# Kernel optimization log

Hardware: AMD Instinct MI355X
Metric: run time of the kernel (lower is better)

## Reference

```python
import jax, jax.numpy as jnp
import numpy as np

B, T, E, H = 2, 1024, 1024, 16
HD = E // H
TEMP = 0.5


def setup_inputs() -> dict:
    key = jax.random.key(0)
    ks = jax.random.split(key, 20)
    d = {
        "query1": jax.random.normal(ks[0], (B, T, E), jnp.float32),
        "query2": jax.random.normal(ks[1], (B, T, E), jnp.float32),
        "key": jax.random.normal(ks[2], (B, T, E), jnp.float32),
        "value": jax.random.normal(ks[3], (B, T, E), jnp.float32),
    }
    s = 1.0 / np.sqrt(E)
    names = ["Wq", "Wq2", "Wq3", "Wk", "Wv", "Wo"]
    for i, n in enumerate(names):
        d[n] = jax.random.normal(ks[4 + i], (E, E), jnp.float32) * s
        d["b" + n[1:]] = jax.random.normal(ks[10 + i], (E,), jnp.float32) * 0.01
    return d


def _heads(x):
    # [B,T,E] -> [B,H,T,HD]
    b, t, _ = x.shape
    return x.reshape(b, t, H, HD).transpose(0, 2, 1, 3)


def reference(query1, query2, key, value,
              Wq, bq, Wq2, bq2, Wq3, bq3, Wk, bk, Wv, bv, Wo, bo):
    q = _heads(query1 @ Wq.T + bq)
    q2 = _heads(query2 @ Wq2.T + bq2)
    q3 = _heads(key @ Wq3.T + bq3)
    k = _heads(key @ Wk.T + bk)
    v = _heads(value @ Wv.T + bv)
    b, _, t, _ = q.shape
    scale = 1.0 / np.sqrt(HD)

    def global_attn(qx):
        s = jnp.einsum('bhtd,bhsd->bhts', qx, k) * scale  # [B,H,T,T]
        # global softmax over flattened T*T, temperature-scaled, times T
        a = jax.nn.softmax((s / TEMP).reshape(b, H, t * t), axis=-1)
        return a.reshape(b, H, t, t) * t

    a1 = global_attn(q)
    a2 = global_attn(q2)
    a3 = global_attn(q3)
    attn_out = jnp.einsum('bhts,bhsd->bthd', (a1 + a2 + a3) / 3.0, v)
    attn_out = attn_out.reshape(b, t, E)
    output = attn_out @ Wo.T + bo
    return output, a1
```

## Files before the change

kernel.cpp:

```cpp
#include <hip/hip_runtime.h>
#include <hip/hip_bf16.h>


#define B_ 2
#define T_ 1024
#define E_ 1024
#define H_ 16
#define HD_ 64
#define BH_ 32

typedef float f32x4 __attribute__((ext_vector_type(4)));
typedef short bfrag __attribute__((ext_vector_type(8)));

__device__ __forceinline__ unsigned short f2b(float f) {
  unsigned int u = __float_as_uint(f);
  u += 0x7fffu + ((u >> 16) & 1u);
  return (unsigned short)(u >> 16);
}

struct CvtArgs { const float* src[10]; unsigned short* dst[10]; int n[10]; };

__global__ __launch_bounds__(256) void cvt_kernel(CvtArgs a) {
  const int z = blockIdx.y;
  const float* __restrict__ s = a.src[z];
  unsigned short* __restrict__ d = a.dst[z];
  const int n = a.n[z];
  const int stride = gridDim.x * 256 * 4;
  for (int i = (blockIdx.x * 256 + threadIdx.x) * 4; i < n; i += stride) {
    float4 v = *(const float4*)(s + i);
    ushort4 o;
    o.x = f2b(v.x); o.y = f2b(v.y); o.z = f2b(v.z); o.w = f2b(v.w);
    *(ushort4*)(d + i) = o;
  }
}

__device__ __forceinline__ void mm128_core(const unsigned short* __restrict__ A,
                                           const unsigned short* __restrict__ W,
                                           int m0, int n0,
                                           unsigned short* As, unsigned short* Bs,
                                           f32x4 acc[4][4]) {
  const int tid  = threadIdx.x;
  const int lane = tid & 63, w = tid >> 6;
  const int lrow = lane & 15, quad = lane >> 4;
  const int wm = (w >> 1) * 64, wn = (w & 1) * 64;
  const int srow = tid >> 2, soff = (tid & 3) * 8;

  const unsigned short* Ar0 = A + (size_t)(m0 + srow) * E_ + soff;
  const unsigned short* Ar1 = Ar0 + (size_t)64 * E_;
  const unsigned short* Br0 = W + (size_t)(n0 + srow) * E_ + soff;
  const unsigned short* Br1 = Br0 + (size_t)64 * E_;

  for (int k0 = 0; k0 < E_; k0 += 32) {
    int4 a0 = *(const int4*)(Ar0 + k0);
    int4 a1 = *(const int4*)(Ar1 + k0);
    int4 b0 = *(const int4*)(Br0 + k0);
    int4 b1 = *(const int4*)(Br1 + k0);
    __syncthreads();
    *(int4*)(As + srow * 32 + soff)        = a0;
    *(int4*)(As + (srow + 64) * 32 + soff) = a1;
    *(int4*)(Bs + srow * 32 + soff)        = b0;
    *(int4*)(Bs + (srow + 64) * 32 + soff) = b1;
    __syncthreads();
    bfrag af[4], bf_[4];
#pragma unroll
    for (int mt = 0; mt < 4; mt++)
      af[mt] = *(const bfrag*)(As + (wm + mt * 16 + lrow) * 32 + quad * 8);
#pragma unroll
    for (int nt = 0; nt < 4; nt++)
      bf_[nt] = *(const bfrag*)(Bs + (wn + nt * 16 + lrow) * 32 + quad * 8);
#pragma unroll
    for (int mt = 0; mt < 4; mt++)
#pragma unroll
      for (int nt = 0; nt < 4; nt++)
        acc[mt][nt] = __builtin_amdgcn_mfma_f32_16x16x32_bf16(af[mt], bf_[nt], acc[mt][nt], 0, 0, 0);
  }
}

struct ProjArgs {
  const unsigned short* X[5];
  const unsigned short* W[5];
  const float* bias[5];
  unsigned short* dst[5];
};

__global__ __launch_bounds__(256) void proj_kernel(ProjArgs pa) {
  __shared__ unsigned short As[128 * 32];
  __shared__ unsigned short Bs[128 * 32];
  const int z = blockIdx.z;
  const int m0 = blockIdx.y * 128, n0 = blockIdx.x * 128;
  f32x4 acc[4][4];
#pragma unroll
  for (int mt = 0; mt < 4; mt++)
#pragma unroll
    for (int nt = 0; nt < 4; nt++) acc[mt][nt] = (f32x4)0.f;

  mm128_core(pa.X[z], pa.W[z], m0, n0, As, Bs, acc);

  const int tid = threadIdx.x, lane = tid & 63, w = tid >> 6;
  const int lrow = lane & 15, quad = lane >> 4;
  const int wm = (w >> 1) * 64, wn = (w & 1) * 64;
  const float* __restrict__ bias = pa.bias[z];
  unsigned short* __restrict__ dst = pa.dst[z];
  float bv[4];
#pragma unroll
  for (int nt = 0; nt < 4; nt++) bv[nt] = bias[n0 + wn + nt * 16 + lrow];
#pragma unroll
  for (int mt = 0; mt < 4; mt++)
#pragma unroll
    for (int nt = 0; nt < 4; nt++)
#pragma unroll
      for (int ii = 0; ii < 4; ii++) {
        const int m = m0 + wm + mt * 16 + quad * 4 + ii;
        const int n = n0 + wn + nt * 16 + lrow;
        const float v = acc[mt][nt][ii] + bv[nt];
        const int b = m >> 10, t = m & 1023, h = n >> 6, dd = n & 63;
        size_t idx;
        if (z == 4)
          idx = ((size_t)((b * H_ + h) * HD_ + dd)) * T_ + t;
        else
          idx = ((size_t)((b * H_ + h) * T_ + t)) * HD_ + dd;
        dst[idx] = f2b(v);
      }
}

__global__ __launch_bounds__(256) void attn_sums_kernel(
    const unsigned short* __restrict__ Q1, const unsigned short* __restrict__ Q2,
    const unsigned short* __restrict__ Q3, const unsigned short* __restrict__ Kh,
    float* __restrict__ sums) {
  const int tid = threadIdx.x, lane = tid & 63, w = tid >> 6;
  const int lrow = lane & 15, quad = lane >> 4;
  const int tw = w >> 1, sw = w & 1;
  const int bh = blockIdx.y;
  const int tb = blockIdx.x * 128 + tw * 64;
  const size_t base = (size_t)bh * T_ * HD_;
  const unsigned short* Qs[3] = {Q1 + base, Q2 + base, Q3 + base};
  const unsigned short* Kb = Kh + base;

  float lsum[3] = {0.f, 0.f, 0.f};
  for (int s0 = 0; s0 < T_; s0 += 128) {
    const int sb = s0 + sw * 64;
#pragma unroll
    for (int i = 0; i < 3; i++) {
      f32x4 acc[4][4];
#pragma unroll
      for (int mt = 0; mt < 4; mt++)
#pragma unroll
        for (int nt = 0; nt < 4; nt++) acc[mt][nt] = (f32x4)0.f;
#pragma unroll
      for (int kk = 0; kk < 2; kk++) {
        bfrag af[4], bf_[4];
#pragma unroll
        for (int mt = 0; mt < 4; mt++)
          af[mt] = *(const bfrag*)(Qs[i] + (size_t)(tb + mt * 16 + lrow) * HD_ + kk * 32 + quad * 8);
#pragma unroll
        for (int nt = 0; nt < 4; nt++)
          bf_[nt] = *(const bfrag*)(Kb + (size_t)(sb + nt * 16 + lrow) * HD_ + kk * 32 + quad * 8);
#pragma unroll
        for (int mt = 0; mt < 4; mt++)
#pragma unroll
          for (int nt = 0; nt < 4; nt++)
            acc[mt][nt] = __builtin_amdgcn_mfma_f32_16x16x32_bf16(af[mt], bf_[nt], acc[mt][nt], 0, 0, 0);
      }
      float s = 0.f;
#pragma unroll
      for (int mt = 0; mt < 4; mt++)
#pragma unroll
        for (int nt = 0; nt < 4; nt++)
#pragma unroll
          for (int ii = 0; ii < 4; ii++)
            s += __expf(acc[mt][nt][ii] * 0.25f);
      lsum[i] += s;
    }
  }
#pragma unroll
  for (int i = 0; i < 3; i++) {
    float v = lsum[i];
    for (int off = 32; off > 0; off >>= 1) v += __shfl_down(v, off, 64);
    if (lane == 0) atomicAdd(&sums[i * BH_ + bh], v);
  }
}

__global__ __launch_bounds__(256) void attn_main_kernel(
    const unsigned short* __restrict__ Q1, const unsigned short* __restrict__ Q2,
    const unsigned short* __restrict__ Q3, const unsigned short* __restrict__ Kh,
    const unsigned short* __restrict__ Vt, const float* __restrict__ sums,
    float* __restrict__ a1out, unsigned short* __restrict__ attn_out) {
  __shared__ unsigned short P[128 * 136];
  const int tid = threadIdx.x, lane = tid & 63, w = tid >> 6;
  const int lrow = lane & 15, quad = lane >> 4;
  const int tw = w >> 1, sw = w & 1, dw = sw;
  const int bh = blockIdx.y;
  const int b = bh >> 4, h = bh & 15;
  const int tb = blockIdx.x * 128 + tw * 64;
  const size_t base = (size_t)bh * T_ * HD_;
  const unsigned short* Qs[3] = {Q1 + base, Q2 + base, Q3 + base};
  const unsigned short* Kb = Kh + base;
  const unsigned short* Vb = Vt + (size_t)bh * HD_ * T_;

  float r[3];
#pragma unroll
  for (int i = 0; i < 3; i++) r[i] = (float)T_ / (3.f * sums[i * BH_ + bh]);
  const float a1s = 3.f * r[0];

  f32x4 oacc[4][2];
#pragma unroll
  for (int mt = 0; mt < 4; mt++) { oacc[mt][0] = (f32x4)0.f; oacc[mt][1] = (f32x4)0.f; }

  for (int s0 = 0; s0 < T_; s0 += 128) {
    const int sb = s0 + sw * 64;
    f32x4 pc[4][4];
#pragma unroll
    for (int mt = 0; mt < 4; mt++)
#pragma unroll
      for (int nt = 0; nt < 4; nt++) pc[mt][nt] = (f32x4)0.f;

#pragma unroll
    for (int i = 0; i < 3; i++) {
      f32x4 acc[4][4];
#pragma unroll
      for (int mt = 0; mt < 4; mt++)
#pragma unroll
        for (int nt = 0; nt < 4; nt++) acc[mt][nt] = (f32x4)0.f;
#pragma unroll
      for (int kk = 0; kk < 2; kk++) {
        bfrag af[4], bf_[4];
#pragma unroll
        for (int mt = 0; mt < 4; mt++)
          af[mt] = *(const bfrag*)(Qs[i] + (size_t)(tb + mt * 16 + lrow) * HD_ + kk * 32 + quad * 8);
#pragma unroll
        for (int nt = 0; nt < 4; nt++)
          bf_[nt] = *(const bfrag*)(Kb + (size_t)(sb + nt * 16 + lrow) * HD_ + kk * 32 + quad * 8);
#pragma unroll
        for (int mt = 0; mt < 4; mt++)
#pragma unroll
          for (int nt = 0; nt < 4; nt++)
            acc[mt][nt] = __builtin_amdgcn_mfma_f32_16x16x32_bf16(af[mt], bf_[nt], acc[mt][nt], 0, 0, 0);
      }
      const float ri = r[i];
#pragma unroll
      for (int mt = 0; mt < 4; mt++)
#pragma unroll
        for (int nt = 0; nt < 4; nt++)
#pragma unroll
          for (int ii = 0; ii < 4; ii++) {
            const float e = __expf(acc[mt][nt][ii] * 0.25f);
            pc[mt][nt][ii] += ri * e;
            if (i == 0) {
              const int t = tb + mt * 16 + quad * 4 + ii;
              const int s = sb + nt * 16 + lrow;
              a1out[((size_t)bh * T_ + t) * T_ + s] = e * a1s;
            }
          }
    }
    __syncthreads();
#pragma unroll
    for (int mt = 0; mt < 4; mt++)
#pragma unroll
      for (int nt = 0; nt < 4; nt++)
#pragma unroll
        for (int ii = 0; ii < 4; ii++) {
          const int tl = tw * 64 + mt * 16 + quad * 4 + ii;
          const int sl = sw * 64 + nt * 16 + lrow;
          P[tl * 136 + sl] = f2b(pc[mt][nt][ii]);
        }
    __syncthreads();
#pragma unroll
    for (int kk = 0; kk < 4; kk++) {
      bfrag pf[4], vf[2];
#pragma unroll
      for (int mt = 0; mt < 4; mt++)
        pf[mt] = *(const bfrag*)(P + (tw * 64 + mt * 16 + lrow) * 136 + kk * 32 + quad * 8);
#pragma unroll
      for (int nt = 0; nt < 2; nt++)
        vf[nt] = *(const bfrag*)(Vb + (size_t)(dw * 32 + nt * 16 + lrow) * T_ + s0 + kk * 32 + quad * 8);
#pragma unroll
      for (int mt = 0; mt < 4; mt++)
#pragma unroll
        for (int nt = 0; nt < 2; nt++)
          oacc[mt][nt] = __builtin_amdgcn_mfma_f32_16x16x32_bf16(pf[mt], vf[nt], oacc[mt][nt], 0, 0, 0);
    }
  }
#pragma unroll
  for (int mt = 0; mt < 4; mt++)
#pragma unroll
    for (int nt = 0; nt < 2; nt++)
#pragma unroll
      for (int ii = 0; ii < 4; ii++) {
        const int t = tb + mt * 16 + quad * 4 + ii;
        const int dd = dw * 32 + nt * 16 + lrow;
        attn_out[((size_t)(b * T_ + t)) * E_ + h * HD_ + dd] = f2b(oacc[mt][nt][ii]);
      }
}

__global__ __launch_bounds__(256) void outproj_kernel(
    const unsigned short* __restrict__ Ab, const unsigned short* __restrict__ Wb,
    const float* __restrict__ bias, float* __restrict__ out) {
  __shared__ unsigned short As[128 * 32];
  __shared__ unsigned short Bs[128 * 32];
  const int m0 = blockIdx.y * 128, n0 = blockIdx.x * 128;
  f32x4 acc[4][4];
#pragma unroll
  for (int mt = 0; mt < 4; mt++)
#pragma unroll
    for (int nt = 0; nt < 4; nt++) acc[mt][nt] = (f32x4)0.f;

  mm128_core(Ab, Wb, m0, n0, As, Bs, acc);

  const int tid = threadIdx.x, lane = tid & 63, w = tid >> 6;
  const int lrow = lane & 15, quad = lane >> 4;
  const int wm = (w >> 1) * 64, wn = (w & 1) * 64;
  float bv[4];
#pragma unroll
  for (int nt = 0; nt < 4; nt++) bv[nt] = bias[n0 + wn + nt * 16 + lrow];
#pragma unroll
  for (int mt = 0; mt < 4; mt++)
#pragma unroll
    for (int nt = 0; nt < 4; nt++)
#pragma unroll
      for (int ii = 0; ii < 4; ii++) {
        const int m = m0 + wm + mt * 16 + quad * 4 + ii;
        const int n = n0 + wn + nt * 16 + lrow;
        out[(size_t)m * E_ + n] = acc[mt][nt][ii] + bv[nt];
      }
}

extern "C" void kernel_launch(void* const* d_in, const int* in_sizes, int n_in,
                              void* d_out, int out_size, void* d_ws, size_t ws_size,
                              hipStream_t stream) {
  const float* q1f  = (const float*)d_in[0];
  const float* q2f  = (const float*)d_in[1];
  const float* keyf = (const float*)d_in[2];
  const float* valf = (const float*)d_in[3];
  const float* Wq  = (const float*)d_in[4];  const float* bq  = (const float*)d_in[5];
  const float* Wq2 = (const float*)d_in[6];  const float* bq2 = (const float*)d_in[7];
  const float* Wq3 = (const float*)d_in[8];  const float* bq3 = (const float*)d_in[9];
  const float* Wk  = (const float*)d_in[10]; const float* bk  = (const float*)d_in[11];
  const float* Wv  = (const float*)d_in[12]; const float* bv  = (const float*)d_in[13];
  const float* Wo  = (const float*)d_in[14]; const float* bo  = (const float*)d_in[15];

  char* ws = (char*)d_ws;
  const size_t MB = 1024 * 1024;
  unsigned short* xq1  = (unsigned short*)(ws + 0 * MB);
  unsigned short* xq2  = (unsigned short*)(ws + 4 * MB);
  unsigned short* xkey = (unsigned short*)(ws + 8 * MB);
  unsigned short* xval = (unsigned short*)(ws + 12 * MB);
  unsigned short* wq   = (unsigned short*)(ws + 16 * MB);
  unsigned short* wq2  = (unsigned short*)(ws + 18 * MB);
  unsigned short* wq3  = (unsigned short*)(ws + 20 * MB);
  unsigned short* wk   = (unsigned short*)(ws + 22 * MB);
  unsigned short* wv   = (unsigned short*)(ws + 24 * MB);
  unsigned short* wo   = (unsigned short*)(ws + 26 * MB);
  unsigned short* Qh1  = (unsigned short*)(ws + 28 * MB);
  unsigned short* Qh2  = (unsigned short*)(ws + 32 * MB);
  unsigned short* Qh3  = (unsigned short*)(ws + 36 * MB);
  unsigned short* Kh   = (unsigned short*)(ws + 40 * MB);
  unsigned short* Vt   = (unsigned short*)(ws + 44 * MB);
  unsigned short* attn = (unsigned short*)(ws + 48 * MB);
  float* sums          = (float*)(ws + 52 * MB);

  CvtArgs ca;
  const float* srcs[10] = {q1f, q2f, keyf, valf, Wq, Wq2, Wq3, Wk, Wv, Wo};
  unsigned short* dsts[10] = {xq1, xq2, xkey, xval, wq, wq2, wq3, wk, wv, wo};
  for (int i = 0; i < 10; i++) { ca.src[i] = srcs[i]; ca.dst[i] = dsts[i]; ca.n[i] = (i < 4) ? 2097152 : 1048576; }
  cvt_kernel<<<dim3(2048, 10), 256, 0, stream>>>(ca);

  hipMemsetAsync(sums, 0, 3 * BH_ * sizeof(float), stream);

  ProjArgs pa;
  const unsigned short* Xs[5] = {xq1, xq2, xkey, xkey, xval};
  const unsigned short* Ws_[5] = {wq, wq2, wq3, wk, wv};
  const float* Bi[5] = {bq, bq2, bq3, bk, bv};
  unsigned short* Ds[5] = {Qh1, Qh2, Qh3, Kh, Vt};
  for (int i = 0; i < 5; i++) { pa.X[i] = Xs[i]; pa.W[i] = Ws_[i]; pa.bias[i] = Bi[i]; pa.dst[i] = Ds[i]; }
  proj_kernel<<<dim3(8, 16, 5), 256, 0, stream>>>(pa);

  attn_sums_kernel<<<dim3(8, BH_), 256, 0, stream>>>(Qh1, Qh2, Qh3, Kh, sums);

  float* out = (float*)d_out;
  attn_main_kernel<<<dim3(8, BH_), 256, 0, stream>>>(Qh1, Qh2, Qh3, Kh, Vt, sums,
                                                     out + 2097152, attn);

  outproj_kernel<<<dim3(8, 16), 256, 0, stream>>>(attn, wo, bo, out);
}
```

Before: 372.1 us.

## Use direct global-to-LDS loads, split sums over keys, swizzle blocks, exp2 and nontemporal stores

The GEMM core now stages tiles with global_load_lds instead of a register round trip. The sums kernel splits the key range in two to double its grid, keeps per-lane partial sums, and uses a swizzled block order. The main kernel also swizzles its block order so blocks sharing a head are spread across XCDs. Exponentials switch to exp2f with a folded constant, and the large a1 output is written with nontemporal stores. Several unrelated tweaks are bundled; the LDS layout for direct loads must still match the fragment reads (tid*8 with row stride 32 looks consistent).

```diff
diff --git a/kernel.cpp b/kernel.cpp
--- a/kernel.cpp
+++ b/kernel.cpp
@@ -9,6 +9,8 @@
 #define HD_ 64
 #define BH_ 32
 
+#define CEXP 0.36067376022224085f
+
 typedef float f32x4 __attribute__((ext_vector_type(4)));
 typedef short bfrag __attribute__((ext_vector_type(8)));
 
@@ -16,6 +18,15 @@
   unsigned int u = __float_as_uint(f);
   u += 0x7fffu + ((u >> 16) & 1u);
   return (unsigned short)(u >> 16);
+}
+
+__device__ __forceinline__ void gl_lds16(const unsigned short* g, unsigned short* l) {
+  __builtin_amdgcn_global_load_lds(
+      reinterpret_cast<const __attribute__((address_space(1))) unsigned int*>(
+          reinterpret_cast<uintptr_t>(g)),
+      reinterpret_cast<__attribute__((address_space(3))) unsigned int*>(
+          reinterpret_cast<uintptr_t>(l)),
+      16, 0, 0);
 }
 
 struct CvtArgs { const float* src[10]; unsigned short* dst[10]; int n[10]; };
@@ -49,17 +60,17 @@
   const unsigned short* Ar1 = Ar0 + (size_t)64 * E_;
   const unsigned short* Br0 = W + (size_t)(n0 + srow) * E_ + soff;
   const unsigned short* Br1 = Br0 + (size_t)64 * E_;
+  unsigned short* Ad0 = As + tid * 8;
+  unsigned short* Ad1 = As + 2048 + tid * 8;
+  unsigned short* Bd0 = Bs + tid * 8;
+  unsigned short* Bd1 = Bs + 2048 + tid * 8;
 
   for (int k0 = 0; k0 < E_; k0 += 32) {
-    int4 a0 = *(const int4*)(Ar0 + k0);
-    int4 a1 = *(const int4*)(Ar1 + k0);
-    int4 b0 = *(const int4*)(Br0 + k0);
-    int4 b1 = *(const int4*)(Br1 + k0);
     __syncthreads();
-    *(int4*)(As + srow * 32 + soff)        = a0;
-    *(int4*)(As + (srow + 64) * 32 + soff) = a1;
-    *(int4*)(Bs + srow * 32 + soff)        = b0;
-    *(int4*)(Bs + (srow + 64) * 32 + soff) = b1;
+    gl_lds16(Ar0 + k0, Ad0);
+    gl_lds16(Ar1 + k0, Ad1);
+    gl_lds16(Br0 + k0, Bd0);
+    gl_lds16(Br1 + k0, Bd1);
     __syncthreads();
     bfrag af[4], bf_[4];
 #pragma unroll
@@ -127,18 +138,29 @@
     const unsigned short* __restrict__ Q1, const unsigned short* __restrict__ Q2,
     const unsigned short* __restrict__ Q3, const unsigned short* __restrict__ Kh,
     float* __restrict__ sums) {
+  const int flat = blockIdx.x + 8 * (blockIdx.y + 2 * blockIdx.z);
+  const int swz  = (flat & 7) * 64 + (flat >> 3);
+  const int bx   = swz & 7;
+  const int shalf = (swz >> 3) & 1;
+  const int bh   = swz >> 4;
+
   const int tid = threadIdx.x, lane = tid & 63, w = tid >> 6;
   const int lrow = lane & 15, quad = lane >> 4;
   const int tw = w >> 1, sw = w & 1;
-  const int bh = blockIdx.y;
-  const int tb = blockIdx.x * 128 + tw * 64;
+  const int tb = bx * 128 + tw * 64;
+  const int sbase = shalf * 512;
   const size_t base = (size_t)bh * T_ * HD_;
   const unsigned short* Qs[3] = {Q1 + base, Q2 + base, Q3 + base};
   const unsigned short* Kb = Kh + base;
 
-  float lsum[3] = {0.f, 0.f, 0.f};
-  for (int s0 = 0; s0 < T_; s0 += 128) {
-    const int sb = s0 + sw * 64;
+  float ls[3][4];
+#pragma unroll
+  for (int i = 0; i < 3; i++)
+#pragma unroll
+    for (int ii = 0; ii < 4; ii++) ls[i][ii] = 0.f;
+
+  for (int j = 0; j < 4; j++) {
+    const int sb = sbase + j * 128 + sw * 64;
 #pragma unroll
     for (int i = 0; i < 3; i++) {
       f32x4 acc[4][4];
@@ -161,20 +183,18 @@
           for (int nt = 0; nt < 4; nt++)
             acc[mt][nt] = __builtin_amdgcn_mfma_f32_16x16x32_bf16(af[mt], bf_[nt], acc[mt][nt], 0, 0, 0);
       }
-      float s = 0.f;
 #pragma unroll
       for (int mt = 0; mt < 4; mt++)
 #pragma unroll
         for (int nt = 0; nt < 4; nt++)
 #pragma unroll
           for (int ii = 0; ii < 4; ii++)
-            s += __expf(acc[mt][nt][ii] * 0.25f);
-      lsum[i] += s;
+            ls[i][ii] += exp2f(acc[mt][nt][ii] * CEXP);
     }
   }
 #pragma unroll
   for (int i = 0; i < 3; i++) {
-    float v = lsum[i];
+    float v = (ls[i][0] + ls[i][1]) + (ls[i][2] + ls[i][3]);
     for (int off = 32; off > 0; off >>= 1) v += __shfl_down(v, off, 64);
     if (lane == 0) atomicAdd(&sums[i * BH_ + bh], v);
   }
@@ -186,12 +206,16 @@
     const unsigned short* __restrict__ Vt, const float* __restrict__ sums,
     float* __restrict__ a1out, unsigned short* __restrict__ attn_out) {
   __shared__ unsigned short P[128 * 136];
+  const int flat = blockIdx.x + 8 * blockIdx.y;
+  const int swz  = (flat & 7) * 32 + (flat >> 3);
+  const int bx   = swz & 7;
+  const int bh   = swz >> 3;
+
   const int tid = threadIdx.x, lane = tid & 63, w = tid >> 6;
   const int lrow = lane & 15, quad = lane >> 4;
   const int tw = w >> 1, sw = w & 1, dw = sw;
-  const int bh = blockIdx.y;
   const int b = bh >> 4, h = bh & 15;
-  const int tb = blockIdx.x * 128 + tw * 64;
+  const int tb = bx * 128 + tw * 64;
   const size_t base = (size_t)bh * T_ * HD_;
   const unsigned short* Qs[3] = {Q1 + base, Q2 + base, Q3 + base};
   const unsigned short* Kb = Kh + base;
@@ -243,12 +267,13 @@
         for (int nt = 0; nt < 4; nt++)
 #pragma unroll
           for (int ii = 0; ii < 4; ii++) {
-            const float e = __expf(acc[mt][nt][ii] * 0.25f);
+            const float e = exp2f(acc[mt][nt][ii] * CEXP);
             pc[mt][nt][ii] += ri * e;
             if (i == 0) {
               const int t = tb + mt * 16 + quad * 4 + ii;
               const int s = sb + nt * 16 + lrow;
-              a1out[((size_t)bh * T_ + t) * T_ + s] = e * a1s;
+              __builtin_nontemporal_store(e * a1s,
+                  a1out + ((size_t)bh * T_ + t) * T_ + s);
             }
           }
     }
@@ -374,7 +399,7 @@
   for (int i = 0; i < 5; i++) { pa.X[i] = Xs[i]; pa.W[i] = Ws_[i]; pa.bias[i] = Bi[i]; pa.dst[i] = Ds[i]; }
   proj_kernel<<<dim3(8, 16, 5), 256, 0, stream>>>(pa);
 
-  attn_sums_kernel<<<dim3(8, BH_), 256, 0, stream>>>(Qh1, Qh2, Qh3, Kh, sums);
+  attn_sums_kernel<<<dim3(8, 2, BH_), 256, 0, stream>>>(Qh1, Qh2, Qh3, Kh, sums);
 
   float* out = (float*)d_out;
   attn_main_kernel<<<dim3(8, BH_), 256, 0, stream>>>(Qh1, Qh2, Qh3, Kh, Vt, sums,
```

Result: slower. 394.7 us (+6.1%).
